# Optimization experiments

Hardware: AMD Instinct MI355X
Metric: run time of the kernel (lower is better)

Reference implementation:

```python
import jax, jax.numpy as jnp
import numpy as np

B, T, F = 8, 512, 256
G, V = 2, 8192          # num_codebooks, num_embeddings per group
D = 16
DG = D // G             # per-group codevector dim = 8


def setup_inputs() -> dict:
    key = jax.random.key(0)
    k1, k2, k3, k4, k5 = jax.random.split(key, 5)
    x = jax.random.normal(k1, (B, T, F), dtype=jnp.float32)
    u = jax.random.uniform(k2, (B * T * G, V), dtype=jnp.float32)  # uniform for gumbel
    input_mask = jnp.ones((B, T), dtype=jnp.int32)
    embeddings = jax.random.uniform(k3, (1, G * V, DG), dtype=jnp.float32)
    W_proj = jax.random.normal(k4, (G * V, F), dtype=jnp.float32) * 0.02
    b_proj = jnp.zeros((G * V,), dtype=jnp.float32)
    return {"x": x, "u": u, "embeddings": embeddings,
            "W_proj": W_proj, "b_proj": b_proj, "input_mask": input_mask}


def reference(x, u, embeddings, W_proj, b_proj, input_mask):
    temperature = 1.0
    b, t, _ = x.shape
    # weight projection: [b, t, G*V]
    hidden = jnp.einsum("btf,gf->btg", x, W_proj) + b_proj
    h = hidden.reshape(b * t * G, V)
    # gumbel noise from uniform sample (matches torch.empty().uniform_(tiny, 1))
    tiny = jnp.finfo(h.dtype).tiny
    gumbels = -jnp.log(-jnp.log(jnp.clip(u, tiny, 1.0)))
    codevector_probs = jax.nn.softmax((h + gumbels) / temperature, axis=-1)  # [btG, V]
    # soft distribution (no noise) for perplexity
    soft = jax.nn.softmax(h.reshape(b * t, G, V), axis=-1)
    mask = input_mask.reshape(-1).astype(bool)  # [bt]
    masked = jnp.where(mask[:, None, None], soft, 0.0)
    marginal = masked.sum(0) / input_mask.sum().astype(soft.dtype)  # [G, V]
    perplexity = jnp.exp(-jnp.sum(marginal * jnp.log(marginal + 1e-7), axis=-1)).sum()
    targets_idx = jnp.argmax(codevector_probs, axis=-1).reshape(b, t, G)
    # per-group weighted codebook combination as GEMM (no huge broadcast intermediate)
    pg = codevector_probs.reshape(b * t, G, V)
    emb = embeddings.reshape(G, V, DG)
    codevectors = jnp.einsum("ngv,gvd->ngd", pg, emb).reshape(b, t, G * DG)
    return (codevectors, perplexity, targets_idx)
```

## Files before the change

kernel.cpp:

```cpp
#include <hip/hip_runtime.h>
#include <hip/hip_bf16.h>
#include <math.h>

#define Mrows 4096
#define Kdim  256
#define Ncols 16384
#define Vsz   8192

typedef __attribute__((ext_vector_type(8))) short bf16x8;
typedef __attribute__((ext_vector_type(4))) float f32x4;

__global__ __launch_bounds__(256) void split_bf16(const float* __restrict__ src,
                                                  __hip_bfloat16* __restrict__ hi,
                                                  __hip_bfloat16* __restrict__ lo) {
    const int i = blockIdx.x * 256 + threadIdx.x;
    const float v = src[i];
    const __hip_bfloat16 h = __float2bfloat16(v);
    const float hf = __bfloat162float(h);
    hi[i] = h;
    lo[i] = __float2bfloat16(v - hf);
}

__global__ __launch_bounds__(256) void gemm_mfma(const __hip_bfloat16* __restrict__ Ahi,
                                                 const __hip_bfloat16* __restrict__ Alo,
                                                 const __hip_bfloat16* __restrict__ Bhi,
                                                 const __hip_bfloat16* __restrict__ Blo,
                                                 const float* __restrict__ bias,
                                                 float* __restrict__ hid, int r0) {
    __shared__ unsigned short Ah[128 * 32], Al[128 * 32], Bh[128 * 32], Bl[128 * 32];
    const int tid = threadIdx.x;
    const int lane = tid & 63;
    const int wave = tid >> 6;
    const int bm = blockIdx.x * 128;
    const int bn = blockIdx.y * 128;
    const int wm = (wave & 1) * 64;
    const int wn = (wave >> 1) * 64;
    const int lm = lane & 15;
    const int kq = (lane >> 4) * 8;

    f32x4 acc[4][4];
#pragma unroll
    for (int i = 0; i < 4; ++i)
#pragma unroll
        for (int j = 0; j < 4; ++j) acc[i][j] = (f32x4){0.f, 0.f, 0.f, 0.f};

    for (int k0 = 0; k0 < Kdim; k0 += 32) {
        __syncthreads();
#pragma unroll
        for (int t = 0; t < 2; ++t) {
            const int c = tid + t * 256;
            const int row = c >> 2;
            const int ko = (c & 3) * 8;
            const size_t ga = (size_t)(r0 + bm + row) * Kdim + k0 + ko;
            const size_t gb = (size_t)(bn + row) * Kdim + k0 + ko;
            *(uint4*)&Ah[row * 32 + ko] = *(const uint4*)(Ahi + ga);
            *(uint4*)&Al[row * 32 + ko] = *(const uint4*)(Alo + ga);
            *(uint4*)&Bh[row * 32 + ko] = *(const uint4*)(Bhi + gb);
            *(uint4*)&Bl[row * 32 + ko] = *(const uint4*)(Blo + gb);
        }
        __syncthreads();

        bf16x8 ah[4], al[4], bh[4], bl[4];
#pragma unroll
        for (int i = 0; i < 4; ++i) {
            ah[i] = *(const bf16x8*)&Ah[(wm + i * 16 + lm) * 32 + kq];
            al[i] = *(const bf16x8*)&Al[(wm + i * 16 + lm) * 32 + kq];
            bh[i] = *(const bf16x8*)&Bh[(wn + i * 16 + lm) * 32 + kq];
            bl[i] = *(const bf16x8*)&Bl[(wn + i * 16 + lm) * 32 + kq];
        }
#pragma unroll
        for (int i = 0; i < 4; ++i)
#pragma unroll
            for (int j = 0; j < 4; ++j) {
                acc[i][j] = __builtin_amdgcn_mfma_f32_16x16x32_bf16(ah[i], bh[j], acc[i][j], 0, 0, 0);
                acc[i][j] = __builtin_amdgcn_mfma_f32_16x16x32_bf16(ah[i], bl[j], acc[i][j], 0, 0, 0);
                acc[i][j] = __builtin_amdgcn_mfma_f32_16x16x32_bf16(al[i], bh[j], acc[i][j], 0, 0, 0);
            }
    }

    const int rbase = (lane >> 4) * 4;
#pragma unroll
    for (int j = 0; j < 4; ++j) {
        const int n = bn + wn + j * 16 + lm;
        const float bj = bias[n];
#pragma unroll
        for (int i = 0; i < 4; ++i) {
            const int m0 = bm + wm + i * 16 + rbase;
#pragma unroll
            for (int r2 = 0; r2 < 4; ++r2)
                hid[(size_t)(m0 + r2) * Ncols + n] = acc[i][j][r2] + bj;
        }
    }
}

__global__ __launch_bounds__(256) void phase2(const float* __restrict__ hid,
                                              const float* __restrict__ u,
                                              const float* __restrict__ emb,
                                              const int* __restrict__ mask,
                                              float* __restrict__ marginal,
                                              float* __restrict__ out,
                                              int r0) {
    const int g = blockIdx.y;
    const int n0 = r0 + blockIdx.x * 8;
    const int tid = threadIdx.x;
    const int lane = tid & 63;
    const int wid = tid >> 6;

    __shared__ float marg_s[32 * 256];
    __shared__ float sv1[4]; __shared__ int si1[4]; __shared__ float sv2[4];
    __shared__ float ss1[4], ss2[4], scv[4][8];

#pragma unroll
    for (int i = 0; i < 32; ++i) marg_s[(i << 8) + tid] = 0.f;

    const float* embg = emb + (size_t)g * Vsz * 8;
    float lg[32];

    for (int r = 0; r < 8; ++r) {
        const int n = n0 + r;
        const float* hrow = hid + (size_t)(n - r0) * Ncols + (size_t)g * Vsz;
        const float* urow = u + ((size_t)n * 2 + g) * Vsz;

        float mx1 = -INFINITY, mx2 = -INFINITY;
        int amax = 0;
#pragma unroll
        for (int i = 0; i < 32; ++i) {
            const int v = (i << 8) + tid;
            const float hv = hrow[v];
            float uu = urow[v];
            uu = fminf(fmaxf(uu, 1.17549435e-38f), 1.0f);
            const float d = uu - 1.0f;
            float q = 1.0f / 9.0f;
            q = fmaf(q, d, -0.125f);
            q = fmaf(q, d, 1.0f / 7.0f);
            q = fmaf(q, d, -1.0f / 6.0f);
            q = fmaf(q, d, 0.2f);
            q = fmaf(q, d, -0.25f);
            q = fmaf(q, d, 1.0f / 3.0f);
            q = fmaf(q, d, -0.5f);
            q = fmaf(q, d, 1.0f);
            const float inner = (d > -0.2f) ? (-d) * q : -__logf(uu);
            const float l = hv - __logf(inner);
            lg[i] = l;
            if (l > mx1) { mx1 = l; amax = v; }
            mx2 = fmaxf(mx2, hv);
        }
        float v1 = mx1; int i1 = amax; float v2 = mx2;
#pragma unroll
        for (int off = 32; off > 0; off >>= 1) {
            const float ov = __shfl_down(v1, off);
            const int oi = __shfl_down(i1, off);
            if (ov > v1 || (ov == v1 && oi < i1)) { v1 = ov; i1 = oi; }
            v2 = fmaxf(v2, __shfl_down(v2, off));
        }
        if (lane == 0) { sv1[wid] = v1; si1[wid] = i1; sv2[wid] = v2; }
        __syncthreads();
        if (tid == 0) {
            float bv = sv1[0]; int bi = si1[0]; float b2 = sv2[0];
            for (int w2 = 1; w2 < 4; ++w2) {
                if (sv1[w2] > bv || (sv1[w2] == bv && si1[w2] < bi)) { bv = sv1[w2]; bi = si1[w2]; }
                b2 = fmaxf(b2, sv2[w2]);
            }
            sv1[0] = bv; si1[0] = bi; sv2[0] = b2;
        }
        __syncthreads();
        const float M1 = sv1[0];
        const float M2 = sv2[0];
        const int AMAX = si1[0];

        float s1 = 0.f, s2 = 0.f;
        float cv[8];
#pragma unroll
        for (int d2 = 0; d2 < 8; ++d2) cv[d2] = 0.f;
#pragma unroll
        for (int i = 0; i < 32; ++i) {
            const int v = (i << 8) + tid;
            const float p = __expf(lg[i] - M1);
            s1 += p;
            const float4 e0 = *(const float4*)(embg + (size_t)v * 8);
            const float4 e1 = *(const float4*)(embg + (size_t)v * 8 + 4);
            cv[0] = fmaf(p, e0.x, cv[0]); cv[1] = fmaf(p, e0.y, cv[1]);
            cv[2] = fmaf(p, e0.z, cv[2]); cv[3] = fmaf(p, e0.w, cv[3]);
            cv[4] = fmaf(p, e1.x, cv[4]); cv[5] = fmaf(p, e1.y, cv[5]);
            cv[6] = fmaf(p, e1.z, cv[6]); cv[7] = fmaf(p, e1.w, cv[7]);
            const float qq = __expf(hrow[v] - M2);
            s2 += qq;
            lg[i] = qq;
        }
#pragma unroll
        for (int off = 32; off > 0; off >>= 1) {
            s1 += __shfl_down(s1, off);
            s2 += __shfl_down(s2, off);
        }
#pragma unroll
        for (int d2 = 0; d2 < 8; ++d2)
#pragma unroll
            for (int off = 32; off > 0; off >>= 1) cv[d2] += __shfl_down(cv[d2], off);
        if (lane == 0) {
            ss1[wid] = s1; ss2[wid] = s2;
#pragma unroll
            for (int d2 = 0; d2 < 8; ++d2) scv[wid][d2] = cv[d2];
        }
        __syncthreads();
        if (tid == 0) {
            ss1[0] = ss1[0] + ss1[1] + ss1[2] + ss1[3];
            ss2[0] = ss2[0] + ss2[1] + ss2[2] + ss2[3];
        }
        __syncthreads();
        const float S1 = ss1[0];
        const float S2 = ss2[0];
        if (tid < 8) {
            const float c = scv[0][tid] + scv[1][tid] + scv[2][tid] + scv[3][tid];
            out[(size_t)n * 16 + g * 8 + tid] = c / S1;
        }
        if (tid == 8) out[65537 + (size_t)n * 2 + g] = (float)AMAX;

        if (mask[n] != 0) {
            const float invS2 = 1.0f / S2;
#pragma unroll
            for (int i = 0; i < 32; ++i)
                marg_s[(i << 8) + tid] = fmaf(lg[i], invS2, marg_s[(i << 8) + tid]);
        }
        __syncthreads();
    }
#pragma unroll
    for (int i = 0; i < 32; ++i)
        atomicAdd(&marginal[g * Vsz + (i << 8) + tid], marg_s[(i << 8) + tid]);
}

__global__ __launch_bounds__(256) void ppl_kernel(const float* __restrict__ marginal,
                                                  const int* __restrict__ mask,
                                                  float* __restrict__ out) {
    const int tid = threadIdx.x;
    const int lane = tid & 63;
    const int wid = tid >> 6;
    __shared__ float red[4];
    __shared__ int redi[4];

    int ms = 0;
    for (int i = tid; i < Mrows; i += 256) ms += mask[i];
#pragma unroll
    for (int off = 32; off > 0; off >>= 1) ms += __shfl_down(ms, off);
    if (lane == 0) redi[wid] = ms;
    __syncthreads();
    const float inv = 1.0f / (float)(redi[0] + redi[1] + redi[2] + redi[3]);

    float ppl = 0.f;
    for (int g = 0; g < 2; ++g) {
        float part = 0.f;
        for (int v = tid; v < Vsz; v += 256) {
            const float m = marginal[g * Vsz + v] * inv;
            part += m * logf(m + 1e-7f);
        }
#pragma unroll
        for (int off = 32; off > 0; off >>= 1) part += __shfl_down(part, off);
        __syncthreads();
        if (lane == 0) red[wid] = part;
        __syncthreads();
        if (tid == 0) ppl += __expf(-(red[0] + red[1] + red[2] + red[3]));
        __syncthreads();
    }
    if (tid == 0) out[65536] = ppl;
}

extern "C" void kernel_launch(void* const* d_in, const int* in_sizes, int n_in,
                              void* d_out, int out_size, void* d_ws, size_t ws_size,
                              hipStream_t stream) {
    const float* x    = (const float*)d_in[0];
    const float* u    = (const float*)d_in[1];
    const float* emb  = (const float*)d_in[2];
    const float* w    = (const float*)d_in[3];
    const float* bias = (const float*)d_in[4];
    const int*   mask = (const int*)d_in[5];
    float* out = (float*)d_out;

    char* base = (char*)d_ws;
    float* marginal = (float*)base;
    __hip_bfloat16* Ahi = (__hip_bfloat16*)(base + 65536);
    __hip_bfloat16* Alo = Ahi + 1048576;
    __hip_bfloat16* Bhi = Alo + 1048576;
    __hip_bfloat16* Blo = Bhi + 4194304;
    const size_t hid_off = 65536 + 4194304 + 16777216;
    float* hid = (float*)(base + hid_off);

    size_t cap_rows = (ws_size > hid_off) ? (ws_size - hid_off) / ((size_t)Ncols * 4) : 0;
    int cr = (cap_rows >= Mrows) ? Mrows : (int)((cap_rows / 128) * 128);
    if (cr < 128) cr = 128;

    hipMemsetAsync(marginal, 0, 65536, stream);
    split_bf16<<<4096, 256, 0, stream>>>(x, Ahi, Alo);
    split_bf16<<<16384, 256, 0, stream>>>(w, Bhi, Blo);

    for (int r0 = 0; r0 < Mrows; r0 += cr) {
        const int rows = (Mrows - r0 < cr) ? (Mrows - r0) : cr;
        dim3 gg(rows / 128, Ncols / 128);
        gemm_mfma<<<gg, 256, 0, stream>>>(Ahi, Alo, Bhi, Blo, bias, hid, r0);
        dim3 pg(rows / 8, 2);
        phase2<<<pg, 256, 0, stream>>>(hid, u, emb, mask, marginal, out, r0);
    }
    ppl_kernel<<<1, 256, 0, stream>>>(marginal, mask, out);
}
```

Baseline: 902.0 us.

## Use direct global-to-LDS loads in GEMM and vectorize 512-thread phase2

The GEMM tile loads now use global_load_lds so data goes straight into shared memory without passing through registers. phase2 runs with 512 threads per block, and each thread handles 16 contiguous vocab entries through float4 loads of u and hidden. The hidden values are kept in registers instead of being re-read from global memory. This changes the access pattern from strided to contiguous per thread, which may cause LDS bank conflicts in marg_s, and the larger block may reduce occupancy.

```diff
diff --git a/kernel.cpp b/kernel.cpp
--- a/kernel.cpp
+++ b/kernel.cpp
@@ -11,23 +11,27 @@
 typedef __attribute__((ext_vector_type(4))) float f32x4;
 
 __global__ __launch_bounds__(256) void split_bf16(const float* __restrict__ src,
-                                                  __hip_bfloat16* __restrict__ hi,
-                                                  __hip_bfloat16* __restrict__ lo) {
+                                                  unsigned short* __restrict__ hi,
+                                                  unsigned short* __restrict__ lo) {
     const int i = blockIdx.x * 256 + threadIdx.x;
     const float v = src[i];
     const __hip_bfloat16 h = __float2bfloat16(v);
     const float hf = __bfloat162float(h);
-    hi[i] = h;
-    lo[i] = __float2bfloat16(v - hf);
-}
-
-__global__ __launch_bounds__(256) void gemm_mfma(const __hip_bfloat16* __restrict__ Ahi,
-                                                 const __hip_bfloat16* __restrict__ Alo,
-                                                 const __hip_bfloat16* __restrict__ Bhi,
-                                                 const __hip_bfloat16* __restrict__ Blo,
+    hi[i] = *(const unsigned short*)&h;
+    const __hip_bfloat16 l = __float2bfloat16(v - hf);
+    lo[i] = *(const unsigned short*)&l;
+}
+
+__global__ __launch_bounds__(256) void gemm_mfma(const unsigned short* __restrict__ Ahi,
+                                                 const unsigned short* __restrict__ Alo,
+                                                 const unsigned short* __restrict__ Bhi,
+                                                 const unsigned short* __restrict__ Blo,
                                                  const float* __restrict__ bias,
                                                  float* __restrict__ hid, int r0) {
-    __shared__ unsigned short Ah[128 * 32], Al[128 * 32], Bh[128 * 32], Bl[128 * 32];
+    __shared__ unsigned short sAh[128 * 32];
+    __shared__ unsigned short sAl[128 * 32];
+    __shared__ unsigned short sBh[128 * 32];
+    __shared__ unsigned short sBl[128 * 32];
     const int tid = threadIdx.x;
     const int lane = tid & 63;
     const int wave = tid >> 6;
@@ -38,6 +42,9 @@
     const int lm = lane & 15;
     const int kq = (lane >> 4) * 8;
 
+    const int r_in = lane >> 2;
+    const int k8 = (lane & 3) * 8;
+
     f32x4 acc[4][4];
 #pragma unroll
     for (int i = 0; i < 4; ++i)
@@ -48,25 +55,33 @@
         __syncthreads();
 #pragma unroll
         for (int t = 0; t < 2; ++t) {
-            const int c = tid + t * 256;
-            const int row = c >> 2;
-            const int ko = (c & 3) * 8;
-            const size_t ga = (size_t)(r0 + bm + row) * Kdim + k0 + ko;
-            const size_t gb = (size_t)(bn + row) * Kdim + k0 + ko;
-            *(uint4*)&Ah[row * 32 + ko] = *(const uint4*)(Ahi + ga);
-            *(uint4*)&Al[row * 32 + ko] = *(const uint4*)(Alo + ga);
-            *(uint4*)&Bh[row * 32 + ko] = *(const uint4*)(Bhi + gb);
-            *(uint4*)&Bl[row * 32 + ko] = *(const uint4*)(Blo + gb);
+            const int rbase = wave * 32 + t * 16;
+            const int row = rbase + r_in;
+            const size_t ga = (size_t)(r0 + bm + row) * Kdim + k0 + k8;
+            const size_t gb = (size_t)(bn + row) * Kdim + k0 + k8;
+            const int lds_off = rbase * 32;
+            __builtin_amdgcn_global_load_lds(
+                (const __attribute__((address_space(1))) void*)(Ahi + ga),
+                (__attribute__((address_space(3))) void*)(sAh + lds_off), 16, 0, 0);
+            __builtin_amdgcn_global_load_lds(
+                (const __attribute__((address_space(1))) void*)(Alo + ga),
+                (__attribute__((address_space(3))) void*)(sAl + lds_off), 16, 0, 0);
+            __builtin_amdgcn_global_load_lds(
+                (const __attribute__((address_space(1))) void*)(Bhi + gb),
+                (__attribute__((address_space(3))) void*)(sBh + lds_off), 16, 0, 0);
+            __builtin_amdgcn_global_load_lds(
+                (const __attribute__((address_space(1))) void*)(Blo + gb),
+                (__attribute__((address_space(3))) void*)(sBl + lds_off), 16, 0, 0);
         }
         __syncthreads();
 
         bf16x8 ah[4], al[4], bh[4], bl[4];
 #pragma unroll
         for (int i = 0; i < 4; ++i) {
-            ah[i] = *(const bf16x8*)&Ah[(wm + i * 16 + lm) * 32 + kq];
-            al[i] = *(const bf16x8*)&Al[(wm + i * 16 + lm) * 32 + kq];
-            bh[i] = *(const bf16x8*)&Bh[(wn + i * 16 + lm) * 32 + kq];
-            bl[i] = *(const bf16x8*)&Bl[(wn + i * 16 + lm) * 32 + kq];
+            ah[i] = *(const bf16x8*)&sAh[(wm + i * 16 + lm) * 32 + kq];
+            al[i] = *(const bf16x8*)&sAl[(wm + i * 16 + lm) * 32 + kq];
+            bh[i] = *(const bf16x8*)&sBh[(wn + i * 16 + lm) * 32 + kq];
+            bl[i] = *(const bf16x8*)&sBl[(wn + i * 16 + lm) * 32 + kq];
         }
 #pragma unroll
         for (int i = 0; i < 4; ++i)
@@ -78,14 +93,14 @@
             }
     }
 
-    const int rbase = (lane >> 4) * 4;
+    const int rbase2 = (lane >> 4) * 4;
 #pragma unroll
     for (int j = 0; j < 4; ++j) {
         const int n = bn + wn + j * 16 + lm;
         const float bj = bias[n];
 #pragma unroll
         for (int i = 0; i < 4; ++i) {
-            const int m0 = bm + wm + i * 16 + rbase;
+            const int m0 = bm + wm + i * 16 + rbase2;
 #pragma unroll
             for (int r2 = 0; r2 < 4; ++r2)
                 hid[(size_t)(m0 + r2) * Ncols + n] = acc[i][j][r2] + bj;
@@ -93,42 +108,58 @@
     }
 }
 
-__global__ __launch_bounds__(256) void phase2(const float* __restrict__ hid,
-                                              const float* __restrict__ u,
-                                              const float* __restrict__ emb,
-                                              const int* __restrict__ mask,
-                                              float* __restrict__ marginal,
-                                              float* __restrict__ out,
-                                              int r0) {
+__global__ __launch_bounds__(512, 4) void phase2(const float* __restrict__ hid,
+                                                 const float* __restrict__ u,
+                                                 const float* __restrict__ emb,
+                                                 const int* __restrict__ mask,
+                                                 float* __restrict__ marginal,
+                                                 float* __restrict__ out,
+                                                 int r0) {
     const int g = blockIdx.y;
     const int n0 = r0 + blockIdx.x * 8;
     const int tid = threadIdx.x;
     const int lane = tid & 63;
     const int wid = tid >> 6;
 
-    __shared__ float marg_s[32 * 256];
-    __shared__ float sv1[4]; __shared__ int si1[4]; __shared__ float sv2[4];
-    __shared__ float ss1[4], ss2[4], scv[4][8];
-
-#pragma unroll
-    for (int i = 0; i < 32; ++i) marg_s[(i << 8) + tid] = 0.f;
-
+    __shared__ float marg_s[16 * 512];
+    __shared__ float sv1[8]; __shared__ int si1[8]; __shared__ float sv2[8];
+    __shared__ float ss1[8], ss2[8], scv[8][8];
+    __shared__ float sM1, sM2, sS2; __shared__ int sAM;
+
+#pragma unroll
+    for (int j = 0; j < 16; ++j) marg_s[(j << 9) + tid] = 0.f;
+
+    const int vbase = tid * 16;
     const float* embg = emb + (size_t)g * Vsz * 8;
-    float lg[32];
+    float h[16], lg[16];
 
     for (int r = 0; r < 8; ++r) {
         const int n = n0 + r;
-        const float* hrow = hid + (size_t)(n - r0) * Ncols + (size_t)g * Vsz;
-        const float* urow = u + ((size_t)n * 2 + g) * Vsz;
+        const float* hrow = hid + (size_t)(n - r0) * Ncols + (size_t)g * Vsz + vbase;
+        const float* urow = u + ((size_t)n * 2 + g) * Vsz + vbase;
+
+        float4 uv0 = *(const float4*)(urow + 0);
+        float4 uv1 = *(const float4*)(urow + 4);
+        float4 uv2 = *(const float4*)(urow + 8);
+        float4 uv3 = *(const float4*)(urow + 12);
+        float4 hv0 = *(const float4*)(hrow + 0);
+        float4 hv1 = *(const float4*)(hrow + 4);
+        float4 hv2 = *(const float4*)(hrow + 8);
+        float4 hv3 = *(const float4*)(hrow + 12);
+        lg[0] = uv0.x; lg[1] = uv0.y; lg[2] = uv0.z; lg[3] = uv0.w;
+        lg[4] = uv1.x; lg[5] = uv1.y; lg[6] = uv1.z; lg[7] = uv1.w;
+        lg[8] = uv2.x; lg[9] = uv2.y; lg[10] = uv2.z; lg[11] = uv2.w;
+        lg[12] = uv3.x; lg[13] = uv3.y; lg[14] = uv3.z; lg[15] = uv3.w;
+        h[0] = hv0.x; h[1] = hv0.y; h[2] = hv0.z; h[3] = hv0.w;
+        h[4] = hv1.x; h[5] = hv1.y; h[6] = hv1.z; h[7] = hv1.w;
+        h[8] = hv2.x; h[9] = hv2.y; h[10] = hv2.z; h[11] = hv2.w;
+        h[12] = hv3.x; h[13] = hv3.y; h[14] = hv3.z; h[15] = hv3.w;
 
         float mx1 = -INFINITY, mx2 = -INFINITY;
-        int amax = 0;
-#pragma unroll
-        for (int i = 0; i < 32; ++i) {
-            const int v = (i << 8) + tid;
-            const float hv = hrow[v];
-            float uu = urow[v];
-            uu = fminf(fmaxf(uu, 1.17549435e-38f), 1.0f);
+        int am = 0;
+#pragma unroll
+        for (int j = 0; j < 16; ++j) {
+            float uu = fminf(fmaxf(lg[j], 1.17549435e-38f), 1.0f);
             const float d = uu - 1.0f;
             float q = 1.0f / 9.0f;
             q = fmaf(q, d, -0.125f);
@@ -140,12 +171,12 @@
             q = fmaf(q, d, -0.5f);
             q = fmaf(q, d, 1.0f);
             const float inner = (d > -0.2f) ? (-d) * q : -__logf(uu);
-            const float l = hv - __logf(inner);
-            lg[i] = l;
-            if (l > mx1) { mx1 = l; amax = v; }
-            mx2 = fmaxf(mx2, hv);
-        }
-        float v1 = mx1; int i1 = amax; float v2 = mx2;
+            const float l = h[j] - __logf(inner);
+            lg[j] = l;
+            if (l > mx1) { mx1 = l; am = vbase + j; }
+            mx2 = fmaxf(mx2, h[j]);
+        }
+        float v1 = mx1; int i1 = am; float v2 = mx2;
 #pragma unroll
         for (int off = 32; off > 0; off >>= 1) {
             const float ov = __shfl_down(v1, off);
@@ -157,35 +188,34 @@
         __syncthreads();
         if (tid == 0) {
             float bv = sv1[0]; int bi = si1[0]; float b2 = sv2[0];
-            for (int w2 = 1; w2 < 4; ++w2) {
+            for (int w2 = 1; w2 < 8; ++w2) {
                 if (sv1[w2] > bv || (sv1[w2] == bv && si1[w2] < bi)) { bv = sv1[w2]; bi = si1[w2]; }
                 b2 = fmaxf(b2, sv2[w2]);
             }
-            sv1[0] = bv; si1[0] = bi; sv2[0] = b2;
-        }
-        __syncthreads();
-        const float M1 = sv1[0];
-        const float M2 = sv2[0];
-        const int AMAX = si1[0];
+            sM1 = bv; sAM = bi; sM2 = b2;
+        }
+        __syncthreads();
+        const float M1 = sM1;
+        const float M2 = sM2;
 
         float s1 = 0.f, s2 = 0.f;
         float cv[8];
 #pragma unroll
         for (int d2 = 0; d2 < 8; ++d2) cv[d2] = 0.f;
 #pragma unroll
-        for (int i = 0; i < 32; ++i) {
-            const int v = (i << 8) + tid;
-            const float p = __expf(lg[i] - M1);
+        for (int j = 0; j < 16; ++j) {
+            const float p = __expf(lg[j] - M1);
             s1 += p;
-            const float4 e0 = *(const float4*)(embg + (size_t)v * 8);
-            const float4 e1 = *(const float4*)(embg + (size_t)v * 8 + 4);
+            const float* e = embg + (size_t)(vbase + j) * 8;
+            const float4 e0 = *(const float4*)(e);
+            const float4 e1 = *(const float4*)(e + 4);
             cv[0] = fmaf(p, e0.x, cv[0]); cv[1] = fmaf(p, e0.y, cv[1]);
             cv[2] = fmaf(p, e0.z, cv[2]); cv[3] = fmaf(p, e0.w, cv[3]);
             cv[4] = fmaf(p, e1.x, cv[4]); cv[5] = fmaf(p, e1.y, cv[5]);
             cv[6] = fmaf(p, e1.z, cv[6]); cv[7] = fmaf(p, e1.w, cv[7]);
-            const float qq = __expf(hrow[v] - M2);
-            s2 += qq;
-            lg[i] = qq;
+            const float qv = __expf(h[j] - M2);
+            s2 += qv;
+            h[j] = qv;
         }
 #pragma unroll
         for (int off = 32; off > 0; off >>= 1) {
@@ -202,30 +232,29 @@
             for (int d2 = 0; d2 < 8; ++d2) scv[wid][d2] = cv[d2];
         }
         __syncthreads();
-        if (tid == 0) {
-            ss1[0] = ss1[0] + ss1[1] + ss1[2] + ss1[3];
-            ss2[0] = ss2[0] + ss2[1] + ss2[2] + ss2[3];
-        }
-        __syncthreads();
-        const float S1 = ss1[0];
-        const float S2 = ss2[0];
         if (tid < 8) {
-            const float c = scv[0][tid] + scv[1][tid] + scv[2][tid] + scv[3][tid];
+            float c = 0.f, S1 = 0.f;
+            for (int w2 = 0; w2 < 8; ++w2) { c += scv[w2][tid]; S1 += ss1[w2]; }
             out[(size_t)n * 16 + g * 8 + tid] = c / S1;
         }
-        if (tid == 8) out[65537 + (size_t)n * 2 + g] = (float)AMAX;
-
+        if (tid == 8) {
+            float S2 = 0.f;
+            for (int w2 = 0; w2 < 8; ++w2) S2 += ss2[w2];
+            sS2 = S2;
+        }
+        if (tid == 9) out[65537 + (size_t)n * 2 + g] = (float)sAM;
+        __syncthreads();
         if (mask[n] != 0) {
-            const float invS2 = 1.0f / S2;
-#pragma unroll
-            for (int i = 0; i < 32; ++i)
-                marg_s[(i << 8) + tid] = fmaf(lg[i], invS2, marg_s[(i << 8) + tid]);
-        }
-        __syncthreads();
-    }
-#pragma unroll
-    for (int i = 0; i < 32; ++i)
-        atomicAdd(&marginal[g * Vsz + (i << 8) + tid], marg_s[(i << 8) + tid]);
+            const float invS2 = 1.0f / sS2;
+#pragma unroll
+            for (int j = 0; j < 16; ++j)
+                marg_s[(j << 9) + tid] = fmaf(h[j], invS2, marg_s[(j << 9) + tid]);
+        }
+        __syncthreads();
+    }
+#pragma unroll
+    for (int j = 0; j < 16; ++j)
+        atomicAdd(&marginal[g * Vsz + vbase + j], marg_s[(j << 9) + tid]);
 }
 
 __global__ __launch_bounds__(256) void ppl_kernel(const float* __restrict__ marginal,
@@ -276,10 +305,10 @@
 
     char* base = (char*)d_ws;
     float* marginal = (float*)base;
-    __hip_bfloat16* Ahi = (__hip_bfloat16*)(base + 65536);
-    __hip_bfloat16* Alo = Ahi + 1048576;
-    __hip_bfloat16* Bhi = Alo + 1048576;
-    __hip_bfloat16* Blo = Bhi + 4194304;
+    unsigned short* Ahi = (unsigned short*)(base + 65536);
+    unsigned short* Alo = Ahi + 1048576;
+    unsigned short* Bhi = Alo + 1048576;
+    unsigned short* Blo = Bhi + 4194304;
     const size_t hid_off = 65536 + 4194304 + 16777216;
     float* hid = (float*)(base + hid_off);
 
@@ -296,7 +325,7 @@
         dim3 gg(rows / 128, Ncols / 128);
         gemm_mfma<<<gg, 256, 0, stream>>>(Ahi, Alo, Bhi, Blo, bias, hid, r0);
         dim3 pg(rows / 8, 2);
-        phase2<<<pg, 256, 0, stream>>>(hid, u, emb, mask, marginal, out, r0);
+        phase2<<<pg, 512, 0, stream>>>(hid, u, emb, mask, marginal, out, r0);
     }
     ppl_kernel<<<1, 256, 0, stream>>>(marginal, mask, out);
 }
```

New measurement: 1.174 ms. 30.1% more time.
